# Kernel tuning notes

Hardware: AMD Instinct MI355X
Metric: run time of the kernel (lower is better)

Reference implementation:

```python
import jax, jax.numpy as jnp
import numpy as np
from jax import lax

H = 160; W = 160
D_MODEL = 128; D_INNER = 512; D_STATE = 256; NHEADS = 16; HEADDIM = 32
D_CONV = 4; CHUNK = 64
CONV_DIM = D_INNER + 2 * D_STATE            # 1024
D_IN_PROJ = 2 * D_INNER + 2 * D_STATE + NHEADS  # 1552
EPS = 1e-5


def setup_inputs() -> dict:
    key = jax.random.key(0)
    ks = jax.random.split(key, 8)
    nrm = lambda k, s, sc: jax.random.normal(k, s, jnp.float32) * sc
    return {
        "x": jax.random.normal(ks[0], (1, 3, H, W), jnp.float32),
        "fc0_w": nrm(ks[1], (D_MODEL, 3), 0.3),
        "fc0_b": jnp.zeros((D_MODEL,), jnp.float32),
        "in_proj_w": nrm(ks[2], (D_IN_PROJ, D_MODEL), D_MODEL ** -0.5),
        "conv_w": nrm(ks[3], (CONV_DIM, D_CONV), 0.3),
        "conv_b": jnp.zeros((CONV_DIM,), jnp.float32),
        "dt_bias": jnp.log(jnp.expm1(jax.random.uniform(ks[4], (NHEADS,), minval=0.001, maxval=0.1))),
        "A_log": jnp.log(jax.random.uniform(ks[5], (NHEADS,), minval=1.0, maxval=16.0)),
        "D": jnp.ones((NHEADS,), jnp.float32),
        "norm_w": jnp.ones((D_INNER,), jnp.float32),
        "out_proj_w": nrm(ks[6], (D_MODEL, D_INNER), D_INNER ** -0.5),
        "fc1_w": nrm(ks[7], (D_MODEL, H * W), (H * W) ** -0.5),
        "fc1_b": jnp.zeros((D_MODEL,), jnp.float32),
    }


def segsum(x):
    # x: (..., T) -> (..., T, T) with out[i,j] = sum_{j < d <= i} x[d], -inf above diag
    T = x.shape[-1]
    strict = jnp.tril(jnp.ones((T, T), dtype=bool), -1)
    xx = jnp.where(strict, x[..., :, None], 0.0)
    cs = jnp.cumsum(xx, axis=-2)
    keep = jnp.tril(jnp.ones((T, T), dtype=bool))
    return jnp.where(keep, cs, -jnp.inf)


def ssd(xh, A, Bm, Cm):
    # xh: (b,l,h,p) already multiplied by dt; A: (b,l,h) = dt*A_head; Bm,Cm: (b,l,n) (ngroups=1)
    b, l, h, p = xh.shape
    n = Bm.shape[-1]
    c, q = l // CHUNK, CHUNK
    xh = xh.reshape(b, c, q, h, p)
    A = A.reshape(b, c, q, h).transpose(0, 3, 1, 2)          # (b,h,c,q)
    Bm = Bm.reshape(b, c, q, n)
    Cm = Cm.reshape(b, c, q, n)
    A_cs = jnp.cumsum(A, axis=-1)                            # (b,h,c,q)
    Lmat = jnp.exp(segsum(A))                                # (b,h,c,q,q)
    # intra-chunk (quadratic attention-like) term
    Y_diag = jnp.einsum('bcln,bcsn,bhcls,bcshp->bclhp', Cm, Bm, Lmat, xh)
    # per-chunk final states
    decay = jnp.exp(A_cs[..., -1:] - A_cs)                   # (b,h,c,q)
    states = jnp.einsum('bcln,bhcl,bclhp->bchpn', Bm, decay, xh)
    # inter-chunk recurrence: state entering each chunk
    a_tot = jnp.exp(A_cs[..., -1])                           # (b,h,c)
    def step(carry, inp):
        a_c, s_c = inp                                       # (b,h), (b,h,p,n)
        return a_c[..., None, None] * carry + s_c, carry
    _, states_in = lax.scan(step, jnp.zeros((b, h, p, n), xh.dtype),
                            (jnp.moveaxis(a_tot, 2, 0), jnp.moveaxis(states, 1, 0)))
    states_in = jnp.moveaxis(states_in, 0, 1)                # (b,c,h,p,n)
    Y_off = jnp.einsum('bcln,bchpn,bhcl->bclhp', Cm, states_in, jnp.exp(A_cs))
    return (Y_diag + Y_off).reshape(b, l, h, p)


def _forward(x, fc0_w, fc0_b, in_proj_w, conv_w, conv_b, dt_bias, A_log, D,
             norm_w, out_proj_w, fc1_w, fc1_b):
    b = x.shape[0]
    hw = H * W
    # bidirectional pixel flattening
    x1 = x.transpose(0, 2, 3, 1).reshape(b, hw, 3)
    x2 = x[:, :, ::-1, ::-1].transpose(0, 2, 3, 1).reshape(b, hw, 3)
    xc = jnp.concatenate([x1, x2], axis=1)                   # (b, 2*hw, 3)
    u = xc @ fc0_w.T + fc0_b                                 # (b, L, 128)
    L = u.shape[1]
    # Mamba2 in_proj
    zxbcdt = u @ in_proj_w.T                                 # (b, L, 1552)
    z = zxbcdt[..., :D_INNER]
    xBC = zxbcdt[..., D_INNER:D_INNER + CONV_DIM]
    dt = jax.nn.softplus(zxbcdt[..., D_INNER + CONV_DIM:] + dt_bias)  # (b, L, 16)
    # causal depthwise conv1d + silu
    conv = lax.conv_general_dilated(xBC.transpose(0, 2, 1), conv_w[:, None, :],
                                    (1,), [(D_CONV - 1, 0)],
                                    feature_group_count=CONV_DIM,
                                    dimension_numbers=('NCH', 'OIH', 'NCH'))
    xBC = jax.nn.silu(conv + conv_b[None, :, None]).transpose(0, 2, 1)
    xh = xBC[..., :D_INNER].reshape(b, L, NHEADS, HEADDIM)
    Bm = xBC[..., D_INNER:D_INNER + D_STATE]
    Cm = xBC[..., D_INNER + D_STATE:]
    A = -jnp.exp(A_log)                                      # (16,)
    Y = ssd(xh * dt[..., None], dt * A, Bm, Cm)
    Y = Y + D[None, None, :, None] * xh                      # skip connection
    y = Y.reshape(b, L, D_INNER)
    # gated RMSNorm (norm_before_gate=False)
    y = y * jax.nn.silu(z)
    y = y * lax.rsqrt(jnp.mean(y * y, axis=-1, keepdims=True) + EPS) * norm_w
    out = y @ out_proj_w.T                                   # (b, L, 128)
    # second half of sequence, mean over feature dim (AdaptiveAvgPool1d(1))
    half = out[:, hw:, :].mean(axis=-1)                      # (b, hw)
    return half @ fc1_w.T + fc1_b                            # (b, 128)


def reference(x, fc0_w, fc0_b, in_proj_w, conv_w, conv_b, dt_bias, A_log, D,
              norm_w, out_proj_w, fc1_w, fc1_b):
    return _forward(x, fc0_w, fc0_b, in_proj_w, conv_w, conv_b, dt_bias, A_log,
                    D, norm_w, out_proj_w, fc1_w, fc1_b)
```

## Files before the change

kernel.cpp:

```cpp
#include <hip/hip_runtime.h>

#define H_ 160
#define W_ 160
#define HW 25600
#define L_ 51200
#define DM 128
#define DI 512
#define DS 256
#define NH 16
#define HD 32
#define CONVD 1024
#define DIP 1552
#define NCH 800
#define NCH2 400
#define HPB 8
#define EPSV 1e-5f

typedef __attribute__((ext_vector_type(8))) short bf16x8;
typedef __attribute__((ext_vector_type(8))) unsigned short us8;
typedef __attribute__((ext_vector_type(4))) unsigned short us4;
typedef __attribute__((ext_vector_type(4))) float f32x4;
#define MFMA16(a,b,c) __builtin_amdgcn_mfma_f32_16x16x32_bf16(a,b,c,0,0,0)

__device__ __forceinline__ float b2f(unsigned short u){
  union{unsigned int i; float f;} v; v.i = ((unsigned int)u) << 16; return v.f;
}
__device__ __forceinline__ unsigned short f2b(float f){
  union{unsigned int i; float f;} v; v.f = f;
  unsigned int r = v.i + 0x7fffu + ((v.i >> 16) & 1u);
  return (unsigned short)(r >> 16);
}

__global__ void k_coef(const float* __restrict__ opw, const float* __restrict__ nw,
                       float* __restrict__ coef){
  int i = blockIdx.x * blockDim.x + threadIdx.x;
  if (i >= DI) return;
  float s = 0.f;
  for (int j = 0; j < DM; ++j) s += opw[j * DI + i];
  coef[i] = (s / (float)DM) * nw[i];
}

__global__ __launch_bounds__(256) void k_qtab(const float* __restrict__ ipw,
    const float* __restrict__ fw, const float* __restrict__ fb, float* __restrict__ q){
  int j = blockIdx.x * 256 + threadIdx.x;
  if (j >= DIP) return;
  const float* wr = ipw + (size_t)j * DM;
  float s0 = 0.f, s1 = 0.f, s2 = 0.f, sb = 0.f;
  for (int k = 0; k < DM; ++k){
    float w = wr[k];
    s0 += w * fw[k*3+0]; s1 += w * fw[k*3+1]; s2 += w * fw[k*3+2]; sb += w * fb[k];
  }
  reinterpret_cast<float4*>(q)[j] = make_float4(s0, s1, s2, sb);
}

__device__ __forceinline__ void xrow(const float* __restrict__ x, int l, float* o){
  int i, j;
  if (l < HW){ i = l / W_; j = l % W_; }
  else { int l2 = l - HW; i = (H_ - 1) - l2 / W_; j = (W_ - 1) - l2 % W_; }
  int p = i * W_ + j;
  o[0] = x[p]; o[1] = x[HW + p]; o[2] = x[2*HW + p];
}

__global__ __launch_bounds__(256) void k_fused(const float* __restrict__ x,
    const float* __restrict__ q, const float* __restrict__ cw, const float* __restrict__ cb,
    const float* __restrict__ dt_bias,
    unsigned short* __restrict__ g, unsigned short* __restrict__ xbc, float* __restrict__ dtb){
  int r0 = blockIdx.x * 32;
  int tid = threadIdx.x;
  {
    int c8 = tid & 127, lg = tid >> 7;
    const float4* qv8 = reinterpret_cast<const float4*>(q) + DI + c8 * 8;
    const float4* wv8 = reinterpret_cast<const float4*>(cw) + c8 * 8;
    const float4* cb2 = reinterpret_cast<const float4*>(cb) + c8 * 2;
    float4 bias0 = cb2[0], bias1 = cb2[1];
    float biasv[8] = {bias0.x,bias0.y,bias0.z,bias0.w,bias1.x,bias1.y,bias1.z,bias1.w};
    for (int it = 0; it < 4; ++it){
      int lbase = r0 + (it * 2 + lg) * 4;
      float xv[7][3], vf[7];
      #pragma unroll
      for (int k = 0; k < 7; ++k){
        int l = lbase - 3 + k;
        if (l >= 0){ xrow(x, l, xv[k]); vf[k] = 1.f; }
        else { xv[k][0] = xv[k][1] = xv[k][2] = 0.f; vf[k] = 0.f; }
      }
      unsigned int ow[4][4];
      #pragma unroll
      for (int e = 0; e < 8; ++e){
        float4 qv = qv8[e];
        float raw[7];
        #pragma unroll
        for (int k = 0; k < 7; ++k)
          raw[k] = vf[k]*qv.w + xv[k][0]*qv.x + xv[k][1]*qv.y + xv[k][2]*qv.z;
        float4 wv = wv8[e];
        float bias = biasv[e];
        #pragma unroll
        for (int rr = 0; rr < 4; ++rr){
          float acc = bias + raw[rr]*wv.x + raw[rr+1]*wv.y + raw[rr+2]*wv.z + raw[rr+3]*wv.w;
          float s = acc / (1.f + __expf(-acc));
          unsigned int b = f2b(s);
          if (e & 1) ow[rr][e >> 1] |= b << 16;
          else       ow[rr][e >> 1] = b;
        }
      }
      #pragma unroll
      for (int rr = 0; rr < 4; ++rr){
        uint4 o; o.x = ow[rr][0]; o.y = ow[rr][1]; o.z = ow[rr][2]; o.w = ow[rr][3];
        *reinterpret_cast<uint4*>(xbc + (size_t)(lbase + rr) * CONVD + c8 * 8) = o;
      }
    }
  }
  if (r0 >= HW){
    int c8g = tid & 63;
    const float4* qv8 = reinterpret_cast<const float4*>(q) + c8g * 8;
    for (int it = 0; it < 8; ++it){
      int row = it * 4 + (tid >> 6);
      int l = r0 + row;
      float xv[3]; xrow(x, l, xv);
      unsigned int ow[4];
      #pragma unroll
      for (int e = 0; e < 8; ++e){
        float4 qv = qv8[e];
        float raw = qv.w + xv[0]*qv.x + xv[1]*qv.y + xv[2]*qv.z;
        float s = raw / (1.f + __expf(-raw));
        unsigned int b = f2b(s);
        if (e & 1) ow[e >> 1] |= b << 16;
        else       ow[e >> 1] = b;
      }
      uint4 o; o.x = ow[0]; o.y = ow[1]; o.z = ow[2]; o.w = ow[3];
      *reinterpret_cast<uint4*>(g + (size_t)(l - HW) * DI + c8g * 8) = o;
    }
  }
  {
    int row = tid >> 3, h2 = (tid & 7) * 2;
    int l = r0 + row;
    float xv[3]; xrow(x, l, xv);
    #pragma unroll
    for (int e = 0; e < 2; ++e){
      int h = h2 + e;
      float4 qv = reinterpret_cast<const float4*>(q)[DI + CONVD + h];
      float raw = qv.w + xv[0]*qv.x + xv[1]*qv.y + xv[2]*qv.z + dt_bias[h];
      float sp = (raw > 20.f) ? raw : log1pf(__expf(raw));
      dtb[(size_t)l * NH + h] = sp;
    }
  }
}

__global__ __launch_bounds__(256) void k_chunk(const unsigned short* __restrict__ xbc,
    const float* __restrict__ dtb, const float* __restrict__ A_log,
    unsigned short* __restrict__ states, float* __restrict__ atot,
    float* __restrict__ ecs, unsigned short* __restrict__ ydiag, int cbase){
  __shared__ char U[65536];
  __shared__ float dts[64 * HPB];
  __shared__ float Acs[HPB * 64];
  unsigned short* Bs = (unsigned short*)U;
  unsigned short* Cs = (unsigned short*)(U + 32768);
  char* Mb  = U;
  char* xdT = U + 8192;
  char* xwT = U + 12288;
  unsigned short* stageS = (unsigned short*)(U + 16384);
  unsigned short* stageY = (unsigned short*)(U + 33280);
  int cl = blockIdx.x >> 1, hg = blockIdx.x & 1;
  int hbase = hg * HPB;
  int c = cbase + cl, l0 = c * 64;
  int tid = threadIdx.x, lane = tid & 63, wv = tid >> 6;
  int kg = lane >> 4, l15 = lane & 15;
  bool doY = (c >= NCH2);

  for (int i = tid; i < 64 * HPB; i += 256){
    int t = i >> 3, hh = i & 7;
    dts[i] = dtb[(size_t)(l0 + t) * NH + hbase + hh];
  }
  #pragma unroll
  for (int it = 0; it < 8; ++it){
    int r = (tid >> 5) + 8 * it, c8 = tid & 31;
    uint4 v = *reinterpret_cast<const uint4*>(xbc + (size_t)(l0 + r) * CONVD + DI + c8 * 8);
    *reinterpret_cast<uint4*>((char*)Bs + ((r * 512 + c8 * 16) ^ ((r & 7) << 4))) = v;
    if (doY){
      uint4 v2 = *reinterpret_cast<const uint4*>(xbc + (size_t)(l0 + r) * CONVD + DI + DS + c8 * 8);
      *reinterpret_cast<uint4*>((char*)Cs + ((r * 512 + c8 * 16) ^ ((r & 7) << 4))) = v2;
    }
  }
  __syncthreads();
  if (tid < HPB){
    int hh = tid; float Ah = -__expf(A_log[hbase + hh]); float s = 0.f;
    for (int t = 0; t < 64; ++t){ s += dts[t*HPB + hh] * Ah; Acs[hh*64 + t] = s; }
    atot[c * NH + hbase + hh] = __expf(s);
  }
  bf16x8 bst[8];
  #pragma unroll
  for (int nt = 0; nt < 4; ++nt)
    #pragma unroll
    for (int s = 0; s < 2; ++s){
      int n = wv * 64 + nt * 16 + l15;
      int tb = s * 32 + kg * 8;
      bf16x8 f;
      #pragma unroll
      for (int e = 0; e < 8; ++e){
        int t = tb + e;
        f[e] = *reinterpret_cast<const short*>((char*)Bs + ((t * 512 + n * 2) ^ ((t & 7) << 4)));
      }
      bst[nt * 2 + s] = f;
    }
  f32x4 Gacc[4];
  if (doY){
    #pragma unroll
    for (int st = 0; st < 4; ++st) Gacc[st] = (f32x4){0.f,0.f,0.f,0.f};
    int trow = wv * 16 + l15;
    for (int ks = 0; ks < 8; ++ks){
      bf16x8 a = *reinterpret_cast<const bf16x8*>((char*)Cs + ((trow * 512 + (ks*32 + kg*8) * 2) ^ ((trow & 7) << 4)));
      #pragma unroll
      for (int st = 0; st < 4; ++st){
        int srow = st * 16 + l15;
        bf16x8 b = *reinterpret_cast<const bf16x8*>((char*)Bs + ((srow * 512 + (ks*32 + kg*8) * 2) ^ ((srow & 7) << 4)));
        Gacc[st] = MFMA16(a, b, Gacc[st]);
      }
    }
  }
  __syncthreads();
  for (int hh = 0; hh < HPB; ++hh){
    int h = hbase + hh;
    float alast = Acs[hh*64 + 63];
    {
      int t = tid & 63, pb = tid >> 6;
      float dtv = dts[t*HPB + hh];
      float dec = __expf(alast - Acs[hh*64 + t]);
      us8 x8 = *reinterpret_cast<const us8*>(xbc + (size_t)(l0 + t) * CONVD + h * HD + pb * 8);
      #pragma unroll
      for (int e = 0; e < 8; ++e){
        int pp = pb * 8 + e;
        float v = b2f(x8[e]) * dtv;
        if (doY) *reinterpret_cast<unsigned short*>(xdT + ((pp * 128 + t * 2) ^ ((pp & 7) << 4))) = f2b(v);
        *reinterpret_cast<unsigned short*>(xwT + ((pp * 128 + t * 2) ^ ((pp & 7) << 4))) = f2b(v * dec);
      }
    }
    if (doY){
      #pragma unroll
      for (int st = 0; st < 4; ++st)
        #pragma unroll
        for (int r = 0; r < 4; ++r){
          int t = wv * 16 + kg * 4 + r, s2 = st * 16 + l15;
          float m = (s2 <= t) ? Gacc[st][r] * __expf(Acs[hh*64 + t] - Acs[hh*64 + s2]) : 0.f;
          *reinterpret_cast<unsigned short*>(Mb + ((t * 128 + s2 * 2) ^ ((t & 7) << 4))) = f2b(m);
        }
      if (tid < 64) ecs[((size_t)(c - NCH2) * NH + h) * 64 + tid] = __expf(Acs[hh*64 + tid]);
    }
    __syncthreads();
    {
      f32x4 sacc[2][4];
      #pragma unroll
      for (int mt = 0; mt < 2; ++mt)
        #pragma unroll
        for (int nt = 0; nt < 4; ++nt) sacc[mt][nt] = (f32x4){0.f,0.f,0.f,0.f};
      #pragma unroll
      for (int s = 0; s < 2; ++s)
        #pragma unroll
        for (int mt = 0; mt < 2; ++mt){
          int pr = mt * 16 + l15;
          bf16x8 a = *reinterpret_cast<const bf16x8*>(xwT + ((pr * 128 + (s*32 + kg*8) * 2) ^ ((pr & 7) << 4)));
          #pragma unroll
          for (int nt = 0; nt < 4; ++nt) sacc[mt][nt] = MFMA16(a, bst[nt*2 + s], sacc[mt][nt]);
        }
      #pragma unroll
      for (int mt = 0; mt < 2; ++mt)
        #pragma unroll
        for (int nt = 0; nt < 4; ++nt)
          #pragma unroll
          for (int r = 0; r < 4; ++r){
            int pp = mt * 16 + kg * 4 + r, n = wv * 64 + nt * 16 + l15;
            stageS[pp * 264 + n] = f2b(sacc[mt][nt][r]);
          }
    }
    if (doY){
      f32x4 yacc[2];
      yacc[0] = (f32x4){0.f,0.f,0.f,0.f}; yacc[1] = (f32x4){0.f,0.f,0.f,0.f};
      int trow = wv * 16 + l15;
      #pragma unroll
      for (int s = 0; s < 2; ++s){
        bf16x8 a = *reinterpret_cast<const bf16x8*>(Mb + ((trow * 128 + (s*32 + kg*8) * 2) ^ ((trow & 7) << 4)));
        #pragma unroll
        for (int pt = 0; pt < 2; ++pt){
          int pr = pt * 16 + l15;
          bf16x8 b = *reinterpret_cast<const bf16x8*>(xdT + ((pr * 128 + (s*32 + kg*8) * 2) ^ ((pr & 7) << 4)));
          yacc[pt] = MFMA16(a, b, yacc[pt]);
        }
      }
      #pragma unroll
      for (int pt = 0; pt < 2; ++pt)
        #pragma unroll
        for (int r = 0; r < 4; ++r){
          int t = wv * 16 + kg * 4 + r, pp = pt * 16 + l15;
          stageY[t * 40 + pp] = f2b(yacc[pt][r]);
        }
    }
    __syncthreads();
    {
      int row = tid >> 3, seg = tid & 7;
      const unsigned short* sp = stageS + row * 264 + seg * 32;
      unsigned short* gp = states + (((size_t)cl * NH + h) * HD + row) * DS + seg * 32;
      #pragma unroll
      for (int k = 0; k < 4; ++k)
        *reinterpret_cast<uint4*>(gp + k * 8) = *reinterpret_cast<const uint4*>(sp + k * 8);
      if (doY){
        int rw = tid >> 2, quad = tid & 3;
        *reinterpret_cast<uint4*>(ydiag + (size_t)(l0 - HW + rw) * DI + h * HD + quad * 8)
          = *reinterpret_cast<const uint4*>(stageY + rw * 40 + quad * 8);
      }
    }
    __syncthreads();
  }
}

__global__ __launch_bounds__(256) void k_scanred(const unsigned short* __restrict__ states,
    const float* __restrict__ atot, float* __restrict__ carry){
  __shared__ float sat[NCH2];
  int idx = blockIdx.x * 256 + threadIdx.x;
  int h = idx >> 13;
  for (int c = threadIdx.x; c < NCH2; c += 256) sat[c] = atot[c * NH + h];
  __syncthreads();
  float cr = 0.f;
  const unsigned short* p = states + idx;
  for (int c = 0; c < NCH2; ++c){
    cr = sat[c] * cr + b2f(*p);
    p += 131072;
  }
  carry[idx] = cr;
}

__global__ __launch_bounds__(256) void k_scan2(unsigned short* __restrict__ states,
    const float* __restrict__ atot, const float* __restrict__ carry){
  __shared__ float sat[NCH2];
  int idx = blockIdx.x * 256 + threadIdx.x;
  int h = idx >> 13;
  for (int c = threadIdx.x; c < NCH2; c += 256) sat[c] = atot[(NCH2 + c) * NH + h];
  __syncthreads();
  float cr = carry[idx];
  unsigned short* p = states + idx;
  for (int c = 0; c < NCH2; ++c){
    float s = b2f(*p);
    *p = f2b(cr);
    cr = sat[c] * cr + s;
    p += 131072;
  }
}

__global__ __launch_bounds__(256) void k_yoff(const unsigned short* __restrict__ xbc,
    const unsigned short* __restrict__ states, const float* __restrict__ ecs,
    const float* __restrict__ Dv, unsigned short* __restrict__ y,
    const unsigned short* __restrict__ g, float* __restrict__ rms){
  __shared__ unsigned short stage[64 * 520];
  __shared__ float ecs_s[1024];
  int c2 = blockIdx.x;
  int c = c2 + NCH2, l0 = c * 64;
  int tid = threadIdx.x, lane = tid & 63, wv = tid >> 6;
  int kg = lane >> 4, l15 = lane & 15;
  for (int i = tid; i < 1024; i += 256) ecs_s[i] = ecs[(size_t)c2 * 1024 + i];
  bf16x8 aC[8];
  int trow = wv * 16 + l15;
  #pragma unroll
  for (int ks = 0; ks < 8; ++ks)
    aC[ks] = *reinterpret_cast<const bf16x8*>(xbc + (size_t)(l0 + trow) * CONVD + DI + DS + ks * 32 + kg * 8);
  __syncthreads();
  for (int h = 0; h < NH; ++h){
    f32x4 acc[2];
    acc[0] = (f32x4){0.f,0.f,0.f,0.f}; acc[1] = (f32x4){0.f,0.f,0.f,0.f};
    const unsigned short* sb = states + ((size_t)c2 * NH + h) * HD * DS;
    #pragma unroll
    for (int ks = 0; ks < 8; ++ks)
      #pragma unroll
      for (int pt = 0; pt < 2; ++pt){
        bf16x8 b = *reinterpret_cast<const bf16x8*>(sb + (pt * 16 + l15) * DS + ks * 32 + kg * 8);
        acc[pt] = MFMA16(aC[ks], b, acc[pt]);
      }
    float Dh = Dv[h];
    #pragma unroll
    for (int pt = 0; pt < 2; ++pt)
      #pragma unroll
      for (int r = 0; r < 4; ++r){
        int t = wv * 16 + kg * 4 + r, pp = pt * 16 + l15;
        float xh = b2f(xbc[(size_t)(l0 + t) * CONVD + h * HD + pp]);
        stage[t * 520 + h * HD + pp] = f2b(ecs_s[h*64 + t] * acc[pt][r] + Dh * xh);
      }
  }
  __syncthreads();
  int row = tid >> 2, quad = tid & 3;
  const unsigned short* sr = stage + row * 520 + quad * 128;
  size_t obase = (size_t)(c2 * 64 + row) * DI + quad * 128;
  float ss = 0.f;
  #pragma unroll
  for (int k = 0; k < 16; ++k){
    uint4 sv = *reinterpret_cast<const uint4*>(sr + k * 8);
    uint4 yv = *reinterpret_cast<const uint4*>(y + obase + k * 8);
    uint4 gv = *reinterpret_cast<const uint4*>(g + obase + k * 8);
    unsigned int ow[4];
    const unsigned int* svp = (const unsigned int*)&sv;
    const unsigned int* yvp = (const unsigned int*)&yv;
    const unsigned int* gvp = (const unsigned int*)&gv;
    #pragma unroll
    for (int e = 0; e < 4; ++e){
      float v0 = b2f((unsigned short)(svp[e] & 0xffff)) + b2f((unsigned short)(yvp[e] & 0xffff));
      float v1 = b2f((unsigned short)(svp[e] >> 16)) + b2f((unsigned short)(yvp[e] >> 16));
      float y0 = v0 * b2f((unsigned short)(gvp[e] & 0xffff));
      float y1 = v1 * b2f((unsigned short)(gvp[e] >> 16));
      ss += y0 * y0 + y1 * y1;
      ow[e] = (unsigned int)f2b(y0) | ((unsigned int)f2b(y1) << 16);
    }
    uint4 o; o.x = ow[0]; o.y = ow[1]; o.z = ow[2]; o.w = ow[3];
    *reinterpret_cast<uint4*>(y + obase + k * 8) = o;
  }
  ss += __shfl_xor(ss, 1, 64);
  ss += __shfl_xor(ss, 2, 64);
  if (quad == 0) rms[c2 * 64 + row] = rsqrtf(ss / (float)DI + EPSV);
}

__global__ __launch_bounds__(256) void k_half(const unsigned short* __restrict__ yg,
    const float* __restrict__ rms, const float* __restrict__ coef,
    float* __restrict__ half_out){
  int wave = threadIdx.x >> 6, lane = threadIdx.x & 63;
  int row = blockIdx.x * 4 + wave;
  if (row >= HW) return;
  const unsigned short* yr = yg + (size_t)row * DI;
  float acc = 0.f;
  for (int i = lane; i < DI; i += 64) acc += b2f(yr[i]) * coef[i];
  #pragma unroll
  for (int off = 32; off; off >>= 1) acc += __shfl_down(acc, off, 64);
  if (lane == 0) half_out[row] = acc * rms[row];
}

__global__ __launch_bounds__(256) void k_fc1(const float* __restrict__ half_in,
    const float* __restrict__ w, const float* __restrict__ b, float* __restrict__ out){
  int k = blockIdx.x;
  const float* wr = w + (size_t)k * HW;
  float acc = 0.f;
  for (int i = threadIdx.x; i < HW; i += 256) acc += half_in[i] * wr[i];
  __shared__ float red[256];
  red[threadIdx.x] = acc;
  __syncthreads();
  for (int s = 128; s; s >>= 1){
    if (threadIdx.x < s) red[threadIdx.x] += red[threadIdx.x + s];
    __syncthreads();
  }
  if (threadIdx.x == 0) out[k] = red[0] + b[k];
}

extern "C" void kernel_launch(void* const* d_in, const int* in_sizes, int n_in,
                              void* d_out, int out_size, void* d_ws, size_t ws_size,
                              hipStream_t stream){
  const float* x      = (const float*)d_in[0];
  const float* fc0_w  = (const float*)d_in[1];
  const float* fc0_b  = (const float*)d_in[2];
  const float* ipw    = (const float*)d_in[3];
  const float* conv_w = (const float*)d_in[4];
  const float* conv_b = (const float*)d_in[5];
  const float* dt_bias= (const float*)d_in[6];
  const float* A_log  = (const float*)d_in[7];
  const float* Dv     = (const float*)d_in[8];
  const float* norm_w = (const float*)d_in[9];
  const float* opw    = (const float*)d_in[10];
  const float* fc1_w  = (const float*)d_in[11];
  const float* fc1_b  = (const float*)d_in[12];
  float* out = (float*)d_out;

  char* ws = (char*)d_ws;
  size_t off = 0;
  float* dtb          = (float*)(ws + off);           off += (size_t)L_ * NH * 4;
  unsigned short* stx = (unsigned short*)(ws + off);  off += (size_t)L_ * CONVD * 2;
  unsigned short* xbc = (unsigned short*)(ws + off);  off += (size_t)L_ * CONVD * 2;
  unsigned short* g   = (unsigned short*)(ws + off);  off += (size_t)HW * DI * 2;
  unsigned short* yd  = (unsigned short*)(ws + off);  off += (size_t)HW * DI * 2;
  float* atot         = (float*)(ws + off);           off += (size_t)NCH * NH * 4;
  float* ecs          = (float*)(ws + off);           off += (size_t)NCH2 * NH * 64 * 4;
  float* rms          = (float*)(ws + off);           off += (size_t)HW * 4;
  float* half_buf     = (float*)(ws + off);           off += (size_t)HW * 4;
  float* coef         = (float*)(ws + off);           off += (size_t)DI * 4;
  float* carry        = (float*)(ws + off);           off += (size_t)131072 * 4;
  float* qtab         = (float*)(ws + off);           off += (size_t)DIP * 4 * 4;

  if (ws_size < off) return;

  k_coef   <<<2, 256, 0, stream>>>(opw, norm_w, coef);
  k_qtab   <<<(DIP + 255) / 256, 256, 0, stream>>>(ipw, fc0_w, fc0_b, qtab);
  k_fused  <<<L_ / 32, 256, 0, stream>>>(x, qtab, conv_w, conv_b, dt_bias, g, xbc, dtb);
  k_chunk  <<<NCH2 * 2, 256, 0, stream>>>(xbc, dtb, A_log, stx, atot, ecs, yd, 0);
  k_scanred<<<512, 256, 0, stream>>>(stx, atot, carry);
  k_chunk  <<<NCH2 * 2, 256, 0, stream>>>(xbc, dtb, A_log, stx, atot, ecs, yd, NCH2);
  k_scan2  <<<512, 256, 0, stream>>>(stx, atot, carry);
  k_yoff   <<<NCH2, 256, 0, stream>>>(xbc, stx, ecs, Dv, yd, g, rms);
  k_half   <<<HW / 4, 256, 0, stream>>>(yd, rms, coef, half_buf);
  k_fc1    <<<DM, 256, 0, stream>>>(half_buf, fc1_w, fc1_b, out);
}
```

Before: 500.3 us.

## Compute first-half carry state as one decay-weighted contraction instead of per-chunk scan

The carry state entering the second half of the sequence is now computed directly. Each position's x*dt is weighted by its total decay to the halfway point, using chunk prefix sums of dt*A, and then contracted against B. The sum is split into 32 K-slices per head and reduced afterward. This replaces running k_chunk over the first 400 chunks plus a sequential 400-step scan, and lets k_chunk drop its doY branches. The risk is accuracy: weights exp(T - prefix) can underflow or lose precision in bf16, and there is an extra fp32 partial buffer of 16MB aliased onto stx.

After: 501.3 us. About the same (+0.2%).

```diff
diff --git a/kernel.cpp b/kernel.cpp
--- a/kernel.cpp
+++ b/kernel.cpp
@@ -14,6 +14,8 @@
 #define NCH 800
 #define NCH2 400
 #define HPB 8
+#define KSL 32
+#define CPS 13
 #define EPSV 1e-5f
 
 typedef __attribute__((ext_vector_type(8))) short bf16x8;
@@ -145,10 +147,133 @@
   }
 }
 
+__global__ void k_csum(const float* __restrict__ dtb, const float* __restrict__ A_log,
+                       float* __restrict__ Scs){
+  int idx = blockIdx.x * 256 + threadIdx.x;
+  if (idx >= NCH2 * NH) return;
+  int c = idx >> 4, h = idx & 15;
+  float Ah = -__expf(A_log[h]);
+  float s = 0.f;
+  const float* p = dtb + (size_t)c * 64 * NH + h;
+  for (int t = 0; t < 64; ++t) s += p[t * NH];
+  Scs[idx] = s * Ah;
+}
+
+__global__ __launch_bounds__(256) void k_cpre(const float* __restrict__ Scs,
+    float* __restrict__ chunkpre, float* __restrict__ Ttot){
+  __shared__ float segs[256];
+  int tid = threadIdx.x;
+  int h = tid & 15, seg = tid >> 4;
+  int c0 = seg * 25;
+  float v[25];
+  float s = 0.f;
+  #pragma unroll
+  for (int j = 0; j < 25; ++j){ v[j] = Scs[(c0 + j) * NH + h]; s += v[j]; }
+  segs[seg * 16 + h] = s;
+  __syncthreads();
+  float excl = 0.f;
+  for (int s2 = 0; s2 < seg; ++s2) excl += segs[s2 * 16 + h];
+  float run = excl;
+  #pragma unroll
+  for (int j = 0; j < 25; ++j){ chunkpre[(c0 + j) * NH + h] = run; run += v[j]; }
+  if (seg == 15) Ttot[h] = run;
+}
+
+__global__ __launch_bounds__(256) void k_carry(const unsigned short* __restrict__ xbc,
+    const float* __restrict__ dtb, const float* __restrict__ A_log,
+    const float* __restrict__ chunkpre, const float* __restrict__ Ttot,
+    float* __restrict__ part){
+  __shared__ char U[37120];
+  unsigned short* Bs = (unsigned short*)U;
+  char* xwT = U + 32768;
+  float* wcs = (float*)(U + 36864);
+  int h = blockIdx.x & 15, ks = blockIdx.x >> 4;
+  int tid = threadIdx.x, lane = tid & 63, wv = tid >> 6;
+  int kg = lane >> 4, l15 = lane & 15;
+  int c0 = ks * CPS, cend = min(c0 + CPS, NCH2);
+  float Ah = -__expf(A_log[h]);
+  float Tt = Ttot[h];
+  f32x4 sacc[2][4];
+  #pragma unroll
+  for (int mt = 0; mt < 2; ++mt)
+    #pragma unroll
+    for (int nt = 0; nt < 4; ++nt) sacc[mt][nt] = (f32x4){0.f,0.f,0.f,0.f};
+  for (int c = c0; c < cend; ++c){
+    int l0 = c * 64;
+    __syncthreads();
+    #pragma unroll
+    for (int it = 0; it < 8; ++it){
+      int r = (tid >> 5) + 8 * it, c8 = tid & 31;
+      uint4 v = *reinterpret_cast<const uint4*>(xbc + (size_t)(l0 + r) * CONVD + DI + c8 * 8);
+      *reinterpret_cast<uint4*>((char*)Bs + ((r * 512 + c8 * 16) ^ ((r & 7) << 4))) = v;
+    }
+    if (wv == 0){
+      float d = dtb[(size_t)(l0 + lane) * NH + h] * Ah;
+      #pragma unroll
+      for (int off = 1; off < 64; off <<= 1){
+        float o = __shfl_up(d, off, 64);
+        if (lane >= off) d += o;
+      }
+      wcs[lane] = __expf(Tt - chunkpre[c * NH + h] - d);
+    }
+    __syncthreads();
+    {
+      int t = lane, pb = wv;
+      float w = wcs[t] * dtb[(size_t)(l0 + t) * NH + h];
+      us8 x8 = *reinterpret_cast<const us8*>(xbc + (size_t)(l0 + t) * CONVD + h * HD + pb * 8);
+      #pragma unroll
+      for (int e = 0; e < 8; ++e){
+        int pp = pb * 8 + e;
+        *reinterpret_cast<unsigned short*>(xwT + ((pp * 128 + t * 2) ^ ((pp & 7) << 4))) = f2b(b2f(x8[e]) * w);
+      }
+    }
+    __syncthreads();
+    #pragma unroll
+    for (int s = 0; s < 2; ++s){
+      bf16x8 bfr[4];
+      #pragma unroll
+      for (int nt = 0; nt < 4; ++nt){
+        int n = wv * 64 + nt * 16 + l15;
+        bf16x8 f;
+        #pragma unroll
+        for (int e = 0; e < 8; ++e){
+          int t = s * 32 + kg * 8 + e;
+          f[e] = *reinterpret_cast<const short*>((char*)Bs + ((t * 512 + n * 2) ^ ((t & 7) << 4)));
+        }
+        bfr[nt] = f;
+      }
+      #pragma unroll
+      for (int mt = 0; mt < 2; ++mt){
+        int pr = mt * 16 + l15;
+        bf16x8 a = *reinterpret_cast<const bf16x8*>(xwT + ((pr * 128 + (s*32 + kg*8) * 2) ^ ((pr & 7) << 4)));
+        #pragma unroll
+        for (int nt = 0; nt < 4; ++nt) sacc[mt][nt] = MFMA16(a, bfr[nt], sacc[mt][nt]);
+      }
+    }
+  }
+  float* pb2 = part + ((size_t)(ks * NH + h)) * HD * DS;
+  #pragma unroll
+  for (int mt = 0; mt < 2; ++mt)
+    #pragma unroll
+    for (int nt = 0; nt < 4; ++nt)
+      #pragma unroll
+      for (int r = 0; r < 4; ++r)
+        pb2[(mt * 16 + kg * 4 + r) * DS + wv * 64 + nt * 16 + l15] = sacc[mt][nt][r];
+}
+
+__global__ __launch_bounds__(256) void k_carryred(const float* __restrict__ part,
+                                                  float* __restrict__ carry){
+  int idx = blockIdx.x * 256 + threadIdx.x;
+  float s = 0.f;
+  #pragma unroll 8
+  for (int ks = 0; ks < KSL; ++ks) s += part[(size_t)ks * 131072 + idx];
+  carry[idx] = s;
+}
+
 __global__ __launch_bounds__(256) void k_chunk(const unsigned short* __restrict__ xbc,
     const float* __restrict__ dtb, const float* __restrict__ A_log,
     unsigned short* __restrict__ states, float* __restrict__ atot,
-    float* __restrict__ ecs, unsigned short* __restrict__ ydiag, int cbase){
+    float* __restrict__ ecs, unsigned short* __restrict__ ydiag){
   __shared__ char U[65536];
   __shared__ float dts[64 * HPB];
   __shared__ float Acs[HPB * 64];
@@ -161,10 +286,9 @@
   unsigned short* stageY = (unsigned short*)(U + 33280);
   int cl = blockIdx.x >> 1, hg = blockIdx.x & 1;
   int hbase = hg * HPB;
-  int c = cbase + cl, l0 = c * 64;
+  int c = NCH2 + cl, l0 = c * 64;
   int tid = threadIdx.x, lane = tid & 63, wv = tid >> 6;
   int kg = lane >> 4, l15 = lane & 15;
-  bool doY = (c >= NCH2);
 
   for (int i = tid; i < 64 * HPB; i += 256){
     int t = i >> 3, hh = i & 7;
@@ -175,10 +299,8 @@
     int r = (tid >> 5) + 8 * it, c8 = tid & 31;
     uint4 v = *reinterpret_cast<const uint4*>(xbc + (size_t)(l0 + r) * CONVD + DI + c8 * 8);
     *reinterpret_cast<uint4*>((char*)Bs + ((r * 512 + c8 * 16) ^ ((r & 7) << 4))) = v;
-    if (doY){
-      uint4 v2 = *reinterpret_cast<const uint4*>(xbc + (size_t)(l0 + r) * CONVD + DI + DS + c8 * 8);
-      *reinterpret_cast<uint4*>((char*)Cs + ((r * 512 + c8 * 16) ^ ((r & 7) << 4))) = v2;
-    }
+    uint4 v2 = *reinterpret_cast<const uint4*>(xbc + (size_t)(l0 + r) * CONVD + DI + DS + c8 * 8);
+    *reinterpret_cast<uint4*>((char*)Cs + ((r * 512 + c8 * 16) ^ ((r & 7) << 4))) = v2;
   }
   __syncthreads();
   if (tid < HPB){
@@ -202,7 +324,7 @@
       bst[nt * 2 + s] = f;
     }
   f32x4 Gacc[4];
-  if (doY){
+  {
     #pragma unroll
     for (int st = 0; st < 4; ++st) Gacc[st] = (f32x4){0.f,0.f,0.f,0.f};
     int trow = wv * 16 + l15;
@@ -229,11 +351,11 @@
       for (int e = 0; e < 8; ++e){
         int pp = pb * 8 + e;
         float v = b2f(x8[e]) * dtv;
-        if (doY) *reinterpret_cast<unsigned short*>(xdT + ((pp * 128 + t * 2) ^ ((pp & 7) << 4))) = f2b(v);
+        *reinterpret_cast<unsigned short*>(xdT + ((pp * 128 + t * 2) ^ ((pp & 7) << 4))) = f2b(v);
         *reinterpret_cast<unsigned short*>(xwT + ((pp * 128 + t * 2) ^ ((pp & 7) << 4))) = f2b(v * dec);
       }
     }
-    if (doY){
+    {
       #pragma unroll
       for (int st = 0; st < 4; ++st)
         #pragma unroll
@@ -242,7 +364,7 @@
           float m = (s2 <= t) ? Gacc[st][r] * __expf(Acs[hh*64 + t] - Acs[hh*64 + s2]) : 0.f;
           *reinterpret_cast<unsigned short*>(Mb + ((t * 128 + s2 * 2) ^ ((t & 7) << 4))) = f2b(m);
         }
-      if (tid < 64) ecs[((size_t)(c - NCH2) * NH + h) * 64 + tid] = __expf(Acs[hh*64 + tid]);
+      if (tid < 64) ecs[((size_t)cl * NH + h) * 64 + tid] = __expf(Acs[hh*64 + tid]);
     }
     __syncthreads();
     {
@@ -270,7 +392,7 @@
             stageS[pp * 264 + n] = f2b(sacc[mt][nt][r]);
           }
     }
-    if (doY){
+    {
       f32x4 yacc[2];
       yacc[0] = (f32x4){0.f,0.f,0.f,0.f}; yacc[1] = (f32x4){0.f,0.f,0.f,0.f};
       int trow = wv * 16 + l15;
@@ -300,7 +422,7 @@
       #pragma unroll
       for (int k = 0; k < 4; ++k)
         *reinterpret_cast<uint4*>(gp + k * 8) = *reinterpret_cast<const uint4*>(sp + k * 8);
-      if (doY){
+      {
         int rw = tid >> 2, quad = tid & 3;
         *reinterpret_cast<uint4*>(ydiag + (size_t)(l0 - HW + rw) * DI + h * HD + quad * 8)
           = *reinterpret_cast<const uint4*>(stageY + rw * 40 + quad * 8);
@@ -308,22 +430,6 @@
     }
     __syncthreads();
   }
-}
-
-__global__ __launch_bounds__(256) void k_scanred(const unsigned short* __restrict__ states,
-    const float* __restrict__ atot, float* __restrict__ carry){
-  __shared__ float sat[NCH2];
-  int idx = blockIdx.x * 256 + threadIdx.x;
-  int h = idx >> 13;
-  for (int c = threadIdx.x; c < NCH2; c += 256) sat[c] = atot[c * NH + h];
-  __syncthreads();
-  float cr = 0.f;
-  const unsigned short* p = states + idx;
-  for (int c = 0; c < NCH2; ++c){
-    cr = sat[c] * cr + b2f(*p);
-    p += 131072;
-  }
-  carry[idx] = cr;
 }
 
 __global__ __launch_bounds__(256) void k_scan2(unsigned short* __restrict__ states,
@@ -474,17 +580,23 @@
   float* coef         = (float*)(ws + off);           off += (size_t)DI * 4;
   float* carry        = (float*)(ws + off);           off += (size_t)131072 * 4;
   float* qtab         = (float*)(ws + off);           off += (size_t)DIP * 4 * 4;
+  float* Scs          = (float*)(ws + off);           off += (size_t)NCH2 * NH * 4;
+  float* chunkpre     = (float*)(ws + off);           off += (size_t)NCH2 * NH * 4;
+  float* Ttot         = (float*)(ws + off);           off += (size_t)NH * 4;
+  float* part         = (float*)stx;
 
   if (ws_size < off) return;
 
-  k_coef   <<<2, 256, 0, stream>>>(opw, norm_w, coef);
-  k_qtab   <<<(DIP + 255) / 256, 256, 0, stream>>>(ipw, fc0_w, fc0_b, qtab);
-  k_fused  <<<L_ / 32, 256, 0, stream>>>(x, qtab, conv_w, conv_b, dt_bias, g, xbc, dtb);
-  k_chunk  <<<NCH2 * 2, 256, 0, stream>>>(xbc, dtb, A_log, stx, atot, ecs, yd, 0);
-  k_scanred<<<512, 256, 0, stream>>>(stx, atot, carry);
-  k_chunk  <<<NCH2 * 2, 256, 0, stream>>>(xbc, dtb, A_log, stx, atot, ecs, yd, NCH2);
-  k_scan2  <<<512, 256, 0, stream>>>(stx, atot, carry);
-  k_yoff   <<<NCH2, 256, 0, stream>>>(xbc, stx, ecs, Dv, yd, g, rms);
-  k_half   <<<HW / 4, 256, 0, stream>>>(yd, rms, coef, half_buf);
-  k_fc1    <<<DM, 256, 0, stream>>>(half_buf, fc1_w, fc1_b, out);
-}
+  k_coef    <<<2, 256, 0, stream>>>(opw, norm_w, coef);
+  k_qtab    <<<(DIP + 255) / 256, 256, 0, stream>>>(ipw, fc0_w, fc0_b, qtab);
+  k_fused   <<<L_ / 32, 256, 0, stream>>>(x, qtab, conv_w, conv_b, dt_bias, g, xbc, dtb);
+  k_csum    <<<25, 256, 0, stream>>>(dtb, A_log, Scs);
+  k_cpre    <<<1, 256, 0, stream>>>(Scs, chunkpre, Ttot);
+  k_carry   <<<KSL * NH, 256, 0, stream>>>(xbc, dtb, A_log, chunkpre, Ttot, part);
+  k_carryred<<<512, 256, 0, stream>>>(part, carry);
+  k_chunk   <<<NCH2 * 2, 256, 0, stream>>>(xbc, dtb, A_log, stx, atot, ecs, yd);
+  k_scan2   <<<512, 256, 0, stream>>>(stx, atot, carry);
+  k_yoff    <<<NCH2, 256, 0, stream>>>(xbc, stx, ecs, Dv, yd, g, rms);
+  k_half    <<<HW / 4, 256, 0, stream>>>(yd, rms, coef, half_buf);
+  k_fc1     <<<DM, 256, 0, stream>>>(half_buf, fc1_w, fc1_b, out);
+}
```
